# Optimization experiments

Hardware: AMD Instinct MI355X
Metric: run time of the kernel (lower is better)

## Reference

```python
import jax, jax.numpy as jnp
import numpy as np

N_HEADS = 16
HEAD_DIM = 64
ROPE_BASE = 10000.0


def _rope_cos_sin(T, d, dtype):
    # GPT-NeoX style: inv_freq over even indices, cos/sin duplicated to full head_dim
    inv_freq = 1.0 / (ROPE_BASE ** (jnp.arange(0, d, 2, dtype=jnp.float32) / d))
    freqs = jnp.arange(T, dtype=jnp.float32)[:, None] * inv_freq[None, :]  # [T, d/2]
    emb = jnp.concatenate([freqs, freqs], axis=-1)  # [T, d]
    return jnp.cos(emb).astype(dtype), jnp.sin(emb).astype(dtype)


def _rotate_half(x):
    x1, x2 = jnp.split(x, 2, axis=-1)
    return jnp.concatenate([-x2, x1], axis=-1)


def setup_inputs() -> dict:
    key = jax.random.key(0)
    k1, k2, k3 = jax.random.split(key, 3)
    B, T, C = 2, 2048, 1024
    x = jax.random.normal(k1, (B, T, C), dtype=jnp.float32)
    Wqkv = jax.random.normal(k2, (C, 3 * C), dtype=jnp.float32) * (1.0 / np.sqrt(C))
    Wout = jax.random.normal(k3, (C, C), dtype=jnp.float32) * (1.0 / np.sqrt(C))
    return {"x": x, "Wqkv": Wqkv, "Wout": Wout}


def reference(x, Wqkv, Wout):
    B, T, C = x.shape
    H, D = N_HEADS, HEAD_DIM
    qkv = (x @ Wqkv).reshape(B, T, 3, H, D)
    q, k, v = qkv[:, :, 0], qkv[:, :, 1], qkv[:, :, 2]  # [B,T,H,D]
    q = q.transpose(0, 2, 1, 3)  # [B,H,T,D]
    k = k.transpose(0, 2, 1, 3)
    v = v.transpose(0, 2, 1, 3)
    cos, sin = _rope_cos_sin(T, D, x.dtype)  # [T,D]
    cos = cos[None, None]
    sin = sin[None, None]
    q = q * cos + _rotate_half(q) * sin
    k = k * cos + _rotate_half(k) * sin
    scale = 1.0 / np.sqrt(D)
    scores = jnp.einsum("bhqd,bhkd->bhqk", q, k) * scale  # [B,H,T,T]
    causal = jnp.tril(jnp.ones((T, T), dtype=bool))
    scores = jnp.where(causal[None, None], scores, jnp.finfo(scores.dtype).min)
    attn = jax.nn.softmax(scores, axis=-1)
    out = jnp.einsum("bhqk,bhkd->bhqd", attn, v)  # [B,H,T,D]
    out = out.transpose(0, 2, 1, 3).reshape(B, T, C)
    return out @ Wout
```

## Files before the change

### kernel.cpp

```cpp
#include <hip/hip_runtime.h>


#define B_  2
#define T_  2048
#define C_  1024
#define H_  16
#define D_  64
#define N3_ 3072

typedef unsigned short ushortx8 __attribute__((ext_vector_type(8)));
typedef unsigned short ushortx4 __attribute__((ext_vector_type(4)));
typedef short bf16x8 __attribute__((ext_vector_type(8)));
typedef float f32x4 __attribute__((ext_vector_type(4)));
typedef float f32x16 __attribute__((ext_vector_type(16)));
typedef unsigned int uintx2 __attribute__((ext_vector_type(2)));

__device__ __forceinline__ unsigned short f2bf(float f) {
  union { float f; unsigned u; } v; v.f = f;
  unsigned r = v.u + 0x7FFFu + ((v.u >> 16) & 1u);
  return (unsigned short)(r >> 16);
}
__device__ __forceinline__ float bf2f(unsigned short h) {
  union { unsigned u; float f; } v; v.u = ((unsigned)h) << 16;
  return v.f;
}
__device__ __forceinline__ unsigned cvtpk_bf16(float lo, float hi) {
  unsigned r; asm("v_cvt_pk_bf16_f32 %0, %1, %2" : "=v"(r) : "v"(lo), "v"(hi));
  return r;
}
__device__ __forceinline__ void gload_lds16(const void* g, void* l) {
  __builtin_amdgcn_global_load_lds((const __attribute__((address_space(1))) void*)g,
                                   (__attribute__((address_space(3))) void*)l,
                                   16, 0, 0);
}

__global__ __launch_bounds__(256) void cvt_x_kernel(const float* __restrict__ x,
                                                    unsigned short* __restrict__ xb) {
  size_t i = ((size_t)blockIdx.x * 256 + threadIdx.x) * 4;
  const float4 v = *(const float4*)(x + i);
  ushortx4 o;
  o[0] = f2bf(v.x); o[1] = f2bf(v.y); o[2] = f2bf(v.z); o[3] = f2bf(v.w);
  *(ushortx4*)(xb + i) = o;
}

__global__ __launch_bounds__(256) void tconv_kernel(const float* __restrict__ W,
                                                    unsigned short* __restrict__ WT,
                                                    int K, int N) {
  __shared__ float tile[32][33];
  const int n0 = blockIdx.x * 32, k0 = blockIdx.y * 32;
  const int tx = threadIdx.x & 31, ty = threadIdx.x >> 5;
#pragma unroll
  for (int i = 0; i < 4; ++i)
    tile[ty + i * 8][tx] = W[(size_t)(k0 + ty + i * 8) * N + n0 + tx];
  __syncthreads();
#pragma unroll
  for (int i = 0; i < 4; ++i)
    WT[(size_t)(n0 + ty + i * 8) * K + k0 + tx] = f2bf(tile[tx][ty + i * 8]);
}

template <int OUTF32>
__global__ __launch_bounds__(256) void gemm_bt_kernel(const unsigned short* __restrict__ A,
                                                      const unsigned short* __restrict__ BT,
                                                      void* __restrict__ Cptr,
                                                      int M, int N, int K) {
  __shared__ unsigned short Alds[128 * 64];
  __shared__ unsigned short Blds[128 * 64];
  const int tid = threadIdx.x;
  const int w = tid >> 6, l = tid & 63;
  const int wr = w >> 1, wc = w & 1;
  const int lg = l >> 4, lr = l & 15;
  const int m0 = blockIdx.y * 128, n0 = blockIdx.x * 128;
  const int lr8 = l >> 3;
  const int lc8 = (l & 7) ^ lr8;

  f32x4 acc[4][4];
#pragma unroll
  for (int i = 0; i < 4; ++i)
#pragma unroll
    for (int j = 0; j < 4; ++j) acc[i][j] = f32x4{0.f, 0.f, 0.f, 0.f};

  for (int k0 = 0; k0 < K; k0 += 64) {
    __syncthreads();
#pragma unroll
    for (int i = 0; i < 4; ++i) {
      const int ch = w * 4 + i;
      gload_lds16(A + (size_t)(m0 + ch * 8 + lr8) * K + k0 + lc8 * 8, &Alds[ch * 512]);
      gload_lds16(BT + (size_t)(n0 + ch * 8 + lr8) * K + k0 + lc8 * 8, &Blds[ch * 512]);
    }
    __syncthreads();
#pragma unroll
    for (int kc = 0; kc < 2; ++kc) {
      bf16x8 af[4], bfr[4];
#pragma unroll
      for (int mi = 0; mi < 4; ++mi) {
        const int row = wr * 64 + mi * 16 + lr;
        const int c16 = (kc * 4 + lg) ^ (row & 7);
        af[mi] = *(const bf16x8*)(&Alds[row * 64 + c16 * 8]);
      }
#pragma unroll
      for (int nj = 0; nj < 4; ++nj) {
        const int row = wc * 64 + nj * 16 + lr;
        const int c16 = (kc * 4 + lg) ^ (row & 7);
        bfr[nj] = *(const bf16x8*)(&Blds[row * 64 + c16 * 8]);
      }
#pragma unroll
      for (int mi = 0; mi < 4; ++mi)
#pragma unroll
        for (int nj = 0; nj < 4; ++nj)
          acc[mi][nj] = __builtin_amdgcn_mfma_f32_16x16x32_bf16(af[mi], bfr[nj], acc[mi][nj], 0, 0, 0);
    }
  }
#pragma unroll
  for (int mi = 0; mi < 4; ++mi)
#pragma unroll
    for (int nj = 0; nj < 4; ++nj)
#pragma unroll
      for (int j = 0; j < 4; ++j) {
        const int row = m0 + wr * 64 + mi * 16 + lg * 4 + j;
        const int col = n0 + wc * 64 + nj * 16 + lr;
        if (OUTF32) ((float*)Cptr)[(size_t)row * N + col] = acc[mi][nj][j];
        else ((unsigned short*)Cptr)[(size_t)row * N + col] = f2bf(acc[mi][nj][j]);
      }
}

__global__ __launch_bounds__(256) void rope_pack_kernel(const unsigned short* __restrict__ QKV,
                                                        unsigned short* __restrict__ Qp,
                                                        unsigned short* __restrict__ Kp) {
  const int tt = blockIdx.x, bh = blockIdx.y;
  const int b = bh >> 4, h = bh & 15;
  const int tid = threadIdx.x;
  const int half = tid >> 7;
  const int r = (tid >> 1) & 63;
  const int d0 = (tid & 1) * 16;
  const int t = tt * 64 + r;
  const unsigned short* src = QKV + (size_t)(b * T_ + t) * N3_ + half * C_ + h * D_;
  ushortx8 lo0 = *(const ushortx8*)(src + d0);
  ushortx8 lo1 = *(const ushortx8*)(src + d0 + 8);
  ushortx8 hi0 = *(const ushortx8*)(src + d0 + 32);
  ushortx8 hi1 = *(const ushortx8*)(src + d0 + 40);
  ushortx8 olo0, olo1, ohi0, ohi1;
  const float scale = half ? 1.0f : 0.18033688011112042f;
  const float tf = (float)t;
#pragma unroll
  for (int jj = 0; jj < 16; ++jj) {
    const int d = d0 + jj;
    const float invf = exp2f((float)d * -0.41524101186092036f);
    const float ang = tf * invf;
    const float c = cosf(ang), s = sinf(ang);
    const float xl = bf2f(jj < 8 ? lo0[jj] : lo1[jj - 8]);
    const float xh = bf2f(jj < 8 ? hi0[jj] : hi1[jj - 8]);
    const unsigned short rl = f2bf((xl * c - xh * s) * scale);
    const unsigned short rh = f2bf((xh * c + xl * s) * scale);
    if (jj < 8) { olo0[jj] = rl; ohi0[jj] = rh; }
    else        { olo1[jj - 8] = rl; ohi1[jj - 8] = rh; }
  }
  unsigned short* dst = (half ? Kp : Qp) + ((size_t)bh * T_ + t) * D_;
  *(ushortx8*)(dst + d0) = olo0;
  *(ushortx8*)(dst + d0 + 8) = olo1;
  *(ushortx8*)(dst + d0 + 32) = ohi0;
  *(ushortx8*)(dst + d0 + 40) = ohi1;
}

__global__ __launch_bounds__(256) void vtrans_kernel(const unsigned short* __restrict__ QKV,
                                                     unsigned short* __restrict__ Vt) {
  __shared__ unsigned short tile[64][72];
  const int tt = blockIdx.x, bh = blockIdx.y;
  const int b = bh >> 4, h = bh & 15;
  const int tid = threadIdx.x;
  {
    const int r = tid >> 2, seg = tid & 3;
    const unsigned short* src = QKV + (size_t)(b * T_ + tt * 64 + r) * N3_ + 2 * C_ + h * D_ + seg * 16;
    *(ushortx8*)(&tile[r][seg * 16]) = *(const ushortx8*)(src);
    *(ushortx8*)(&tile[r][seg * 16 + 8]) = *(const ushortx8*)(src + 8);
  }
  __syncthreads();
  {
    const int d = tid >> 2, ts = tid & 3;
    ushortx8 o0, o1;
#pragma unroll
    for (int i = 0; i < 8; ++i) { o0[i] = tile[ts * 16 + i][d]; o1[i] = tile[ts * 16 + 8 + i][d]; }
    unsigned short* dst = Vt + ((size_t)bh * D_ + d) * T_ + tt * 64 + ts * 16;
    *(ushortx8*)(dst) = o0;
    *(ushortx8*)(dst + 8) = o1;
  }
}

__global__ __launch_bounds__(256, 2) void attn6_kernel(const unsigned short* __restrict__ Qp,
                                                       const unsigned short* __restrict__ Kp,
                                                       const unsigned short* __restrict__ Vt,
                                                       unsigned short* __restrict__ Ob) {
  __shared__ unsigned short Klds[2][64 * 64];
  __shared__ unsigned short Vlds[2][64 * 64];
  const int tid = threadIdx.x, w = tid >> 6, l = tid & 63;
  const int lq = l & 31, hi = l >> 5;
  const int swz = lq & 7;
  const int bid = blockIdx.x;
  const int bh = bid & 31;
  const int grp = bid >> 5;
  const int p = (grp < 8) ? (15 - grp) : (grp - 8);
  const int s = 4 * p + w;
  const int q0 = s * 32;
  const int ntiles = 2 * p + 2;
  const size_t koff = (size_t)bh * T_ * D_;
  const unsigned short* Kb = Kp + koff;
  const unsigned short* Vb = Vt + (size_t)bh * D_ * T_;

  const int lr8 = l >> 3;
  const int lc8 = (l & 7) ^ lr8;

  bf16x8 qf[4];
  {
    const unsigned short* qp = Qp + koff + (size_t)(q0 + lq) * D_ + hi * 8;
#pragma unroll
    for (int ds = 0; ds < 4; ++ds) qf[ds] = *(const bf16x8*)(qp + ds * 16);
  }
  f32x16 o0, o1;
#pragma unroll
  for (int r = 0; r < 16; ++r) { o0[r] = 0.f; o1[r] = 0.f; }
  float m = -3.0e38f, lden = 0.f;

#pragma unroll
  for (int i = 0; i < 2; ++i) {
    const int c = w * 2 + i;
    gload_lds16(Kb + (size_t)(c * 8 + lr8) * D_ + lc8 * 8, &Klds[0][c * 512]);
    gload_lds16(Vb + (size_t)(c * 8 + lr8) * T_ + lc8 * 8, &Vlds[0][c * 512]);
  }
  __syncthreads();

  for (int kt = 0; kt < ntiles; ++kt) {
    const int cur = kt & 1;
    if (kt + 1 < ntiles) {
      const int kvn = (kt + 1) * 64;
#pragma unroll
      for (int i = 0; i < 2; ++i) {
        const int c = w * 2 + i;
        gload_lds16(Kb + (size_t)(kvn + c * 8 + lr8) * D_ + lc8 * 8, &Klds[cur ^ 1][c * 512]);
        gload_lds16(Vb + (size_t)(c * 8 + lr8) * T_ + kvn + lc8 * 8, &Vlds[cur ^ 1][c * 512]);
      }
    }
    const int kv0 = kt * 64;
    if (kv0 <= q0 + 31) {
      const unsigned short* KL = &Klds[cur][0];
      const unsigned short* VL = &Vlds[cur][0];
      f32x16 acc0, acc1;
#pragma unroll
      for (int r = 0; r < 16; ++r) { acc0[r] = 0.f; acc1[r] = 0.f; }
      __builtin_amdgcn_s_setprio(1);
#pragma unroll
      for (int ds = 0; ds < 4; ++ds) {
        const int slot = ((ds * 2 + hi) ^ swz) * 8;
        const bf16x8 kf0 = *(const bf16x8*)(&KL[(lq) * 64 + slot]);
        const bf16x8 kf1 = *(const bf16x8*)(&KL[(32 + lq) * 64 + slot]);
        acc0 = __builtin_amdgcn_mfma_f32_32x32x16_bf16(kf0, qf[ds], acc0, 0, 0, 0);
        acc1 = __builtin_amdgcn_mfma_f32_32x32x16_bf16(kf1, qf[ds], acc1, 0, 0, 0);
      }
      __builtin_amdgcn_s_setprio(0);
      if (kv0 + 63 > q0) {
        const int thr0 = q0 + lq - kv0;
        const int thr1 = thr0 - 32;
#pragma unroll
        for (int r = 0; r < 16; ++r) {
          const int kvloc = (r & 3) + 8 * (r >> 2) + 4 * hi;
          if (kvloc > thr0) acc0[r] = -3.0e38f;
          if (kvloc > thr1) acc1[r] = -3.0e38f;
        }
      }
      float mx[8];
#pragma unroll
      for (int i = 0; i < 8; ++i)
        mx[i] = fmaxf(fmaxf(acc0[i], acc0[i + 8]), fmaxf(acc1[i], acc1[i + 8]));
#pragma unroll
      for (int i = 0; i < 4; ++i) mx[i] = fmaxf(mx[i], mx[i + 4]);
      const float mloc = fmaxf(fmaxf(mx[0], mx[1]), fmaxf(mx[2], mx[3]));
      const uintx2 mp = __builtin_amdgcn_permlane32_swap(__float_as_uint(mloc), __float_as_uint(mloc), false, false);
      const float pm = fmaxf(__uint_as_float(mp.x), __uint_as_float(mp.y));
      const bool grow = pm > m + 8.0f;
      if (__any(grow)) {
        const float mn = grow ? pm : m;
        const float alpha = __builtin_amdgcn_exp2f(m - mn);
        m = mn;
        lden *= alpha;
#pragma unroll
        for (int r = 0; r < 16; ++r) { o0[r] *= alpha; o1[r] *= alpha; }
      }
      float p0[16], p1[16];
#pragma unroll
      for (int r = 0; r < 16; ++r) {
        p0[r] = __builtin_amdgcn_exp2f(acc0[r] - m);
        p1[r] = __builtin_amdgcn_exp2f(acc1[r] - m);
      }
      unsigned W0 = cvtpk_bf16(p0[0], p0[1]), W1 = cvtpk_bf16(p0[2], p0[3]);
      unsigned W2 = cvtpk_bf16(p0[4], p0[5]), W3 = cvtpk_bf16(p0[6], p0[7]);
      uintx2 Aa = __builtin_amdgcn_permlane32_swap(W0, W2, false, false);
      uintx2 Ab = __builtin_amdgcn_permlane32_swap(W1, W3, false, false);
      union { unsigned u[4]; bf16x8 v; } pfa0 = {{Aa.x, Ab.x, Aa.y, Ab.y}};
      W0 = cvtpk_bf16(p0[8], p0[9]);   W1 = cvtpk_bf16(p0[10], p0[11]);
      W2 = cvtpk_bf16(p0[12], p0[13]); W3 = cvtpk_bf16(p0[14], p0[15]);
      Aa = __builtin_amdgcn_permlane32_swap(W0, W2, false, false);
      Ab = __builtin_amdgcn_permlane32_swap(W1, W3, false, false);
      union { unsigned u[4]; bf16x8 v; } pfa1 = {{Aa.x, Ab.x, Aa.y, Ab.y}};
      W0 = cvtpk_bf16(p1[0], p1[1]);   W1 = cvtpk_bf16(p1[2], p1[3]);
      W2 = cvtpk_bf16(p1[4], p1[5]);   W3 = cvtpk_bf16(p1[6], p1[7]);
      Aa = __builtin_amdgcn_permlane32_swap(W0, W2, false, false);
      Ab = __builtin_amdgcn_permlane32_swap(W1, W3, false, false);
      union { unsigned u[4]; bf16x8 v; } pfb0 = {{Aa.x, Ab.x, Aa.y, Ab.y}};
      W0 = cvtpk_bf16(p1[8], p1[9]);   W1 = cvtpk_bf16(p1[10], p1[11]);
      W2 = cvtpk_bf16(p1[12], p1[13]); W3 = cvtpk_bf16(p1[14], p1[15]);
      Aa = __builtin_amdgcn_permlane32_swap(W0, W2, false, false);
      Ab = __builtin_amdgcn_permlane32_swap(W1, W3, false, false);
      union { unsigned u[4]; bf16x8 v; } pfb1 = {{Aa.x, Ab.x, Aa.y, Ab.y}};

      __builtin_amdgcn_s_setprio(1);
#pragma unroll
      for (int dt = 0; dt < 2; ++dt) {
        const int rowb = (dt * 32 + lq) * 64;
        const bf16x8 vf0 = *(const bf16x8*)(&VL[rowb + ((0 * 2 + hi) ^ swz) * 8]);
        const bf16x8 vf1 = *(const bf16x8*)(&VL[rowb + ((1 * 2 + hi) ^ swz) * 8]);
        const bf16x8 vf2 = *(const bf16x8*)(&VL[rowb + ((2 * 2 + hi) ^ swz) * 8]);
        const bf16x8 vf3 = *(const bf16x8*)(&VL[rowb + ((3 * 2 + hi) ^ swz) * 8]);
        if (dt == 0) {
          o0 = __builtin_amdgcn_mfma_f32_32x32x16_bf16(vf0, pfa0.v, o0, 0, 0, 0);
          o0 = __builtin_amdgcn_mfma_f32_32x32x16_bf16(vf1, pfa1.v, o0, 0, 0, 0);
          o0 = __builtin_amdgcn_mfma_f32_32x32x16_bf16(vf2, pfb0.v, o0, 0, 0, 0);
          o0 = __builtin_amdgcn_mfma_f32_32x32x16_bf16(vf3, pfb1.v, o0, 0, 0, 0);
        } else {
          o1 = __builtin_amdgcn_mfma_f32_32x32x16_bf16(vf0, pfa0.v, o1, 0, 0, 0);
          o1 = __builtin_amdgcn_mfma_f32_32x32x16_bf16(vf1, pfa1.v, o1, 0, 0, 0);
          o1 = __builtin_amdgcn_mfma_f32_32x32x16_bf16(vf2, pfb0.v, o1, 0, 0, 0);
          o1 = __builtin_amdgcn_mfma_f32_32x32x16_bf16(vf3, pfb1.v, o1, 0, 0, 0);
        }
      }
      __builtin_amdgcn_s_setprio(0);
      float sm[8];
#pragma unroll
      for (int i = 0; i < 8; ++i) sm[i] = (p0[i] + p0[i + 8]) + (p1[i] + p1[i + 8]);
#pragma unroll
      for (int i = 0; i < 4; ++i) sm[i] = sm[i] + sm[i + 4];
      const float sloc = (sm[0] + sm[1]) + (sm[2] + sm[3]);
      const uintx2 sp = __builtin_amdgcn_permlane32_swap(__float_as_uint(sloc), __float_as_uint(sloc), false, false);
      lden += __uint_as_float(sp.x) + __uint_as_float(sp.y);
    }
    __syncthreads();
  }

  const float rl = __builtin_amdgcn_rcpf(lden);
  const int b = bh >> 4, hh = bh & 15;
  unsigned short* orow = Ob + (size_t)(b * T_ + q0 + lq) * C_ + hh * D_ + 4 * hi;
#pragma unroll
  for (int rq = 0; rq < 4; ++rq) {
    ushortx4 ov0, ov1;
#pragma unroll
    for (int i = 0; i < 4; ++i) {
      ov0[i] = f2bf(o0[rq * 4 + i] * rl);
      ov1[i] = f2bf(o1[rq * 4 + i] * rl);
    }
    *(ushortx4*)(orow + rq * 8) = ov0;
    *(ushortx4*)(orow + 32 + rq * 8) = ov1;
  }
}

extern "C" void kernel_launch(void* const* d_in, const int* in_sizes, int n_in,
                              void* d_out, int out_size, void* d_ws, size_t ws_size,
                              hipStream_t stream) {
  const float* x = (const float*)d_in[0];
  const float* Wqkv = (const float*)d_in[1];
  const float* Wout = (const float*)d_in[2];
  float* out = (float*)d_out;
  char* ws = (char*)d_ws;
  unsigned short* Xb    = (unsigned short*)(ws);
  unsigned short* WqkvT = (unsigned short*)(ws + (8ull << 20));
  unsigned short* WoutT = (unsigned short*)(ws + (14ull << 20));
  unsigned short* QKVb  = (unsigned short*)(ws + (16ull << 20));
  unsigned short* Qp    = (unsigned short*)(ws + (40ull << 20));
  unsigned short* Kp    = (unsigned short*)(ws + (48ull << 20));
  unsigned short* Vt    = (unsigned short*)(ws + (56ull << 20));
  unsigned short* Ob    = (unsigned short*)(ws + (64ull << 20));

  cvt_x_kernel<<<4096, 256, 0, stream>>>(x, Xb);
  tconv_kernel<<<dim3(N3_ / 32, C_ / 32), 256, 0, stream>>>(Wqkv, WqkvT, C_, N3_);
  tconv_kernel<<<dim3(C_ / 32, C_ / 32), 256, 0, stream>>>(Wout, WoutT, C_, C_);
  gemm_bt_kernel<0><<<dim3(N3_ / 128, (B_ * T_) / 128), 256, 0, stream>>>(
      Xb, WqkvT, QKVb, B_ * T_, N3_, C_);
  rope_pack_kernel<<<dim3(T_ / 64, B_ * H_), 256, 0, stream>>>(QKVb, Qp, Kp);
  vtrans_kernel<<<dim3(T_ / 64, B_ * H_), 256, 0, stream>>>(QKVb, Vt);
  attn6_kernel<<<512, 256, 0, stream>>>(Qp, Kp, Vt, Ob);
  gemm_bt_kernel<1><<<dim3(C_ / 128, (B_ * T_) / 128), 256, 0, stream>>>(
      Ob, WoutT, out, B_ * T_, C_, C_);
}
```

Baseline: 131.0 us.

## Triple-buffer K/V tiles with one barrier and balance causal work per block

Moves the attention K/V staging from double to triple buffering. This cuts the two __syncthreads per tile down to one vmcnt wait plus a single s_barrier, so prefetched loads can stay in flight across the barrier. It also pairs an early and a late query strip inside each block, so every block does a similar amount of causal work instead of blocks ranging from light to heavy. The cost is 50% more LDS per block and a redundant final-tile load, issued so the vmcnt accounting stays uniform.

```diff
diff --git a/kernel.cpp b/kernel.cpp
--- a/kernel.cpp
+++ b/kernel.cpp
@@ -185,22 +185,22 @@
   }
 }
 
-__global__ __launch_bounds__(256, 2) void attn6_kernel(const unsigned short* __restrict__ Qp,
+__global__ __launch_bounds__(256, 2) void attn7_kernel(const unsigned short* __restrict__ Qp,
                                                        const unsigned short* __restrict__ Kp,
                                                        const unsigned short* __restrict__ Vt,
                                                        unsigned short* __restrict__ Ob) {
-  __shared__ unsigned short Klds[2][64 * 64];
-  __shared__ unsigned short Vlds[2][64 * 64];
+  __shared__ unsigned short Klds[3][64 * 64];
+  __shared__ unsigned short Vlds[3][64 * 64];
   const int tid = threadIdx.x, w = tid >> 6, l = tid & 63;
   const int lq = l & 31, hi = l >> 5;
   const int swz = lq & 7;
   const int bid = blockIdx.x;
   const int bh = bid & 31;
-  const int grp = bid >> 5;
-  const int p = (grp < 8) ? (15 - grp) : (grp - 8);
-  const int s = 4 * p + w;
+  const int pp = bid >> 5;
+  const int p = (pp < 8) ? pp : 23 - pp;
+  const int s = (w < 2) ? (2 * p + w) : (62 - 2 * p + (w - 2));
   const int q0 = s * 32;
-  const int ntiles = 2 * p + 2;
+  const int ntiles = 32 - p;
   const size_t koff = (size_t)bh * T_ * D_;
   const unsigned short* Kb = Kp + koff;
   const unsigned short* Vb = Vt + (size_t)bh * D_ * T_;
@@ -225,19 +225,22 @@
     gload_lds16(Kb + (size_t)(c * 8 + lr8) * D_ + lc8 * 8, &Klds[0][c * 512]);
     gload_lds16(Vb + (size_t)(c * 8 + lr8) * T_ + lc8 * 8, &Vlds[0][c * 512]);
   }
-  __syncthreads();
 
   for (int kt = 0; kt < ntiles; ++kt) {
-    const int cur = kt & 1;
-    if (kt + 1 < ntiles) {
-      const int kvn = (kt + 1) * 64;
-#pragma unroll
-      for (int i = 0; i < 2; ++i) {
-        const int c = w * 2 + i;
-        gload_lds16(Kb + (size_t)(kvn + c * 8 + lr8) * D_ + lc8 * 8, &Klds[cur ^ 1][c * 512]);
-        gload_lds16(Vb + (size_t)(c * 8 + lr8) * T_ + kvn + lc8 * 8, &Vlds[cur ^ 1][c * 512]);
-      }
-    }
+    const int cur = kt % 3;
+    const int nxt = (kt + 1) % 3;
+    const int ktn = (kt + 1 < ntiles) ? kt + 1 : kt;
+    const int kvn = ktn * 64;
+#pragma unroll
+    for (int i = 0; i < 2; ++i) {
+      const int c = w * 2 + i;
+      gload_lds16(Kb + (size_t)(kvn + c * 8 + lr8) * D_ + lc8 * 8, &Klds[nxt][c * 512]);
+      gload_lds16(Vb + (size_t)(c * 8 + lr8) * T_ + kvn + lc8 * 8, &Vlds[nxt][c * 512]);
+    }
+    asm volatile("s_waitcnt vmcnt(4)" ::: "memory");
+    __builtin_amdgcn_s_barrier();
+    __builtin_amdgcn_sched_barrier(0);
+
     const int kv0 = kt * 64;
     if (kv0 <= q0 + 31) {
       const unsigned short* KL = &Klds[cur][0];
@@ -340,8 +343,8 @@
       const uintx2 sp = __builtin_amdgcn_permlane32_swap(__float_as_uint(sloc), __float_as_uint(sloc), false, false);
       lden += __uint_as_float(sp.x) + __uint_as_float(sp.y);
     }
-    __syncthreads();
-  }
+  }
+  asm volatile("s_waitcnt vmcnt(0)" ::: "memory");
 
   const float rl = __builtin_amdgcn_rcpf(lden);
   const int b = bh >> 4, hh = bh & 15;
@@ -383,7 +386,7 @@
       Xb, WqkvT, QKVb, B_ * T_, N3_, C_);
   rope_pack_kernel<<<dim3(T_ / 64, B_ * H_), 256, 0, stream>>>(QKVb, Qp, Kp);
   vtrans_kernel<<<dim3(T_ / 64, B_ * H_), 256, 0, stream>>>(QKVb, Vt);
-  attn6_kernel<<<512, 256, 0, stream>>>(Qp, Kp, Vt, Ob);
+  attn7_kernel<<<512, 256, 0, stream>>>(Qp, Kp, Vt, Ob);
   gemm_bt_kernel<1><<<dim3(C_ / 128, (B_ * T_) / 128), 256, 0, stream>>>(
       Ob, WoutT, out, B_ * T_, C_, C_);
 }
```

After: 127.4 us. -2.7%, faster.
